# Performance work log

Measured on AMD Instinct MI355X. Metric: run time of the kernel, lower is better.

Reference implementation:

```python
import jax, jax.numpy as jnp
import numpy as np

D_MODEL = 1024
NUM_HEADS = 16


def setup_inputs() -> dict:
    key = jax.random.key(0)
    ks = jax.random.split(key, 5)
    scale = 1.0 / np.sqrt(D_MODEL)
    X = jax.random.normal(ks[0], (4, 2048, D_MODEL), dtype=jnp.float32)
    W_q = jax.random.normal(ks[1], (D_MODEL, D_MODEL), dtype=jnp.float32) * scale
    W_k = jax.random.normal(ks[2], (D_MODEL, D_MODEL), dtype=jnp.float32) * scale
    W_v = jax.random.normal(ks[3], (D_MODEL, D_MODEL), dtype=jnp.float32) * scale
    W_o = jax.random.normal(ks[4], (D_MODEL, D_MODEL), dtype=jnp.float32) * scale
    return {"X": X, "W_q": W_q, "W_k": W_k, "W_v": W_v, "W_o": W_o}


def reference(X, W_q, W_k, W_v, W_o):
    b, s, d_model = X.shape
    h = NUM_HEADS
    d_k = d_model // h
    # Linear projections (y = x @ W^T convention; W stored as [out,in] would be
    # x @ W.T, but with random weights we use x @ W — math is identical in form).
    def split_heads(y):
        return y.reshape(b, s, h, d_k).transpose(0, 2, 1, 3)  # b h s d
    q = split_heads(X @ W_q)
    k = split_heads(X @ W_k)
    v = split_heads(X @ W_v)
    scores = jnp.einsum('bhid,bhjd->bhij', q, k) / jnp.sqrt(jnp.float32(d_k))
    causal = jnp.tril(jnp.ones((s, s), dtype=bool))
    scores = jnp.where(causal[None, None], scores, jnp.float32(-jnp.inf))
    probs = jax.nn.softmax(scores, axis=-1)
    attended = jnp.einsum('bhij,bhjd->bhid', probs, v)
    out = attended.transpose(0, 2, 1, 3).reshape(b, s, d_model)
    return out @ W_o
```

## Files before the change

kernel.cpp:

```cpp
#include <hip/hip_runtime.h>

typedef __bf16 bf16;
typedef __attribute__((ext_vector_type(8))) __bf16 bf16x8;
typedef __attribute__((ext_vector_type(4))) float f32x4;
typedef __attribute__((ext_vector_type(4))) unsigned short u16x4;

#define D_MODEL 1024
#define SEQ     2048
#define NB      4
#define NH      16
#define DK      64
#define MROWS   (NB * SEQ)

#define MFMA_BF16 __builtin_amdgcn_mfma_f32_16x16x32_bf16
#define EXP2F(x) __builtin_amdgcn_exp2f(x)
#define QSCALE 0.18033688011112042f

__device__ __forceinline__ bf16 f2b(float f) {
    union { float f; unsigned u; } c; c.f = f;
    unsigned r = (c.u + 0x7fffu + ((c.u >> 16) & 1u)) >> 16;
    union { unsigned short s; bf16 b; } o; o.s = (unsigned short)r;
    return o.b;
}
__device__ __forceinline__ unsigned short f2u(float f) {
    union { float f; unsigned u; } c; c.f = f;
    return (unsigned short)((c.u + 0x7fffu + ((c.u >> 16) & 1u)) >> 16);
}
__device__ __forceinline__ unsigned fbits(float f) {
    union { float f; unsigned u; } c; c.f = f; return c.u;
}
__device__ __forceinline__ unsigned pack2(float lo, float hi) {
    return __builtin_amdgcn_perm(fbits(hi), fbits(lo), 0x07060302u);
}

template <int N> struct IC { static constexpr int v = N; };

__global__ void prep_kernel(const float* __restrict__ X,
                            const float* __restrict__ Wq, const float* __restrict__ Wk,
                            const float* __restrict__ Wv, const float* __restrict__ Wo,
                            bf16* __restrict__ Xb, bf16* __restrict__ WqkvT,
                            bf16* __restrict__ WoT) {
    __shared__ float tile[32][33];
    const int bid = blockIdx.x;
    if (bid < 8192) {
        int i = bid * 256 + threadIdx.x;
        float4 v = ((const float4*)X)[i];
        u16x4 o; o[0] = f2u(v.x); o[1] = f2u(v.y); o[2] = f2u(v.z); o[3] = f2u(v.w);
        ((u16x4*)Xb)[i] = o;
    } else {
        int r = bid - 8192;
        int w = r >> 10, tl = r & 1023;
        const float* src = (w == 0) ? Wq : (w == 1) ? Wk : (w == 2) ? Wv : Wo;
        bf16* dst = (w == 3) ? WoT : WqkvT + (size_t)w * 1024 * 1024;
        const int n0 = (tl & 31) * 32, k0 = (tl >> 5) * 32;
        const int tx = threadIdx.x & 31, ty = threadIdx.x >> 5;
#pragma unroll
        for (int i = 0; i < 4; i++)
            tile[ty + i * 8][tx] = src[(size_t)(k0 + ty + i * 8) * 1024 + n0 + tx];
        __syncthreads();
#pragma unroll
        for (int i = 0; i < 4; i++)
            dst[(size_t)(n0 + ty + i * 8) * 1024 + k0 + tx] = f2b(tile[tx][ty + i * 8]);
    }
}

__global__ __launch_bounds__(256) void gemm_qkv(const bf16* __restrict__ A,
                                                const bf16* __restrict__ Bt,
                                                bf16* __restrict__ outQ,
                                                bf16* __restrict__ outV) {
    __shared__ __align__(16) bf16 lA[128 * 64];
    __shared__ __align__(16) bf16 lB[128 * 64];

    const int t = threadIdx.x;
    const int wid = t >> 6, lane = t & 63;
    const int ln = lane & 15, qd = lane >> 4;
    const int wm = wid >> 1, wn = wid & 1;

    const int bid = blockIdx.x;
    const int idx = bid >> 3;
    const int colb = (bid & 7) * 3 + (idx % 3);
    const int rowb = idx / 3;
    const int row0 = rowb * 128, col0 = colb * 128;
    const bool isQK = (col0 < 2048);

    const int srow = t >> 3;
    const int schunk = (t & 7) ^ (srow & 7);
    const bf16* ga = A  + (size_t)(row0 + srow) * 1024 + schunk * 8;
    const bf16* gb = Bt + (size_t)(col0 + srow) * 1024 + schunk * 8;
    const int swk = ln & 7;

    f32x4 acc[4][4];
#pragma unroll
    for (int i = 0; i < 4; i++)
#pragma unroll
        for (int j = 0; j < 4; j++) acc[i][j] = (f32x4){0.f, 0.f, 0.f, 0.f};

    for (int kb = 0; kb < 1024; kb += 64) {
#pragma unroll
        for (int c = 0; c < 4; c++) {
            __builtin_amdgcn_global_load_lds(
                (const __attribute__((address_space(1))) void*)(ga + kb + (size_t)c * 32 * 1024),
                (__attribute__((address_space(3))) void*)(&lA[t * 8 + c * 2048]), 16, 0, 0);
            __builtin_amdgcn_global_load_lds(
                (const __attribute__((address_space(1))) void*)(gb + kb + (size_t)c * 32 * 1024),
                (__attribute__((address_space(3))) void*)(&lB[t * 8 + c * 2048]), 16, 0, 0);
        }
        __syncthreads();

#pragma unroll
        for (int ks = 0; ks < 2; ks++) {
            bf16x8 af[4], bfr[4];
#pragma unroll
            for (int i = 0; i < 4; i++)
                af[i] = *(const bf16x8*)&lA[(wm * 64 + i * 16 + ln) * 64
                                            + ((ks * 4 + qd) ^ swk) * 8];
#pragma unroll
            for (int j = 0; j < 4; j++)
                bfr[j] = *(const bf16x8*)&lB[(wn * 64 + j * 16 + ln) * 64
                                             + ((ks * 4 + qd) ^ swk) * 8];
            if (isQK) {
#pragma unroll
                for (int i = 0; i < 4; i++)
#pragma unroll
                    for (int j = 0; j < 4; j++)
                        acc[i][j] = MFMA_BF16(bfr[j], af[i], acc[i][j], 0, 0, 0);
            } else {
#pragma unroll
                for (int i = 0; i < 4; i++)
#pragma unroll
                    for (int j = 0; j < 4; j++)
                        acc[i][j] = MFMA_BF16(af[i], bfr[j], acc[i][j], 0, 0, 0);
            }
        }
        __syncthreads();
    }

    if (isQK) {
#pragma unroll
        for (int i = 0; i < 4; i++)
#pragma unroll
            for (int j = 0; j < 4; j++) {
                int m  = row0 + wm * 64 + i * 16 + ln;
                int n0 = col0 + wn * 64 + j * 16 + qd * 4;
                float scale = (n0 < 1024) ? QSCALE : 1.0f;
                int b = m >> 11, s = m & 2047;
                int h = (n0 & 1023) >> 6, d0 = n0 & 63;
                size_t addr = (((size_t)(b * NH + h) * SEQ + s) * DK + d0)
                              + (size_t)(n0 >> 10) * 8388608;
                u16x4 w;
#pragma unroll
                for (int r = 0; r < 4; r++) w[r] = f2u(acc[i][j][r] * scale);
                *(u16x4*)&outQ[addr] = w;
            }
    } else {
#pragma unroll
        for (int i = 0; i < 4; i++)
#pragma unroll
            for (int j = 0; j < 4; j++) {
                int m0 = row0 + wm * 64 + i * 16 + qd * 4;
                int n  = col0 + wn * 64 + j * 16 + ln - 2048;
                int b = m0 >> 11, s0 = m0 & 2047;
                int h = n >> 6, d = n & 63;
                size_t addr = ((size_t)(b * NH + h) * DK + d) * SEQ + s0;
                u16x4 w;
#pragma unroll
                for (int r = 0; r < 4; r++) w[r] = f2u(acc[i][j][r]);
                *(u16x4*)&outV[addr] = w;
            }
    }
}

__global__ __launch_bounds__(256) void gemm_o(const bf16* __restrict__ A,
                                              const bf16* __restrict__ Bt,
                                              float* __restrict__ out) {
    __shared__ __align__(16) bf16 lA[128 * 64];
    __shared__ __align__(16) bf16 lB[128 * 64];

    const int t = threadIdx.x;
    const int wid = t >> 6, lane = t & 63;
    const int ln = lane & 15, qd = lane >> 4;
    const int wm = wid >> 1, wn = wid & 1;

    const int bid = blockIdx.x;
    const int colb = bid & 7, rowb = bid >> 3;
    const int row0 = rowb * 128, col0 = colb * 128;

    const int srow = t >> 3;
    const int schunk = (t & 7) ^ (srow & 7);
    const bf16* ga = A  + (size_t)(row0 + srow) * 1024 + schunk * 8;
    const bf16* gb = Bt + (size_t)(col0 + srow) * 1024 + schunk * 8;
    const int swk = ln & 7;

    f32x4 acc[4][4];
#pragma unroll
    for (int i = 0; i < 4; i++)
#pragma unroll
        for (int j = 0; j < 4; j++) acc[i][j] = (f32x4){0.f, 0.f, 0.f, 0.f};

    for (int kb = 0; kb < 1024; kb += 64) {
#pragma unroll
        for (int c = 0; c < 4; c++) {
            __builtin_amdgcn_global_load_lds(
                (const __attribute__((address_space(1))) void*)(ga + kb + (size_t)c * 32 * 1024),
                (__attribute__((address_space(3))) void*)(&lA[t * 8 + c * 2048]), 16, 0, 0);
            __builtin_amdgcn_global_load_lds(
                (const __attribute__((address_space(1))) void*)(gb + kb + (size_t)c * 32 * 1024),
                (__attribute__((address_space(3))) void*)(&lB[t * 8 + c * 2048]), 16, 0, 0);
        }
        __syncthreads();

#pragma unroll
        for (int ks = 0; ks < 2; ks++) {
            bf16x8 af[4], bfr[4];
#pragma unroll
            for (int i = 0; i < 4; i++)
                af[i] = *(const bf16x8*)&lA[(wm * 64 + i * 16 + ln) * 64
                                            + ((ks * 4 + qd) ^ swk) * 8];
#pragma unroll
            for (int j = 0; j < 4; j++)
                bfr[j] = *(const bf16x8*)&lB[(wn * 64 + j * 16 + ln) * 64
                                             + ((ks * 4 + qd) ^ swk) * 8];
#pragma unroll
            for (int i = 0; i < 4; i++)
#pragma unroll
                for (int j = 0; j < 4; j++)
                    acc[i][j] = MFMA_BF16(bfr[j], af[i], acc[i][j], 0, 0, 0);
        }
        __syncthreads();
    }

#pragma unroll
    for (int i = 0; i < 4; i++)
#pragma unroll
        for (int j = 0; j < 4; j++) {
            int m  = row0 + wm * 64 + i * 16 + ln;
            int n0 = col0 + wn * 64 + j * 16 + qd * 4;
            *(f32x4*)&out[(size_t)m * 1024 + n0] = acc[i][j];
        }
}

__global__ __launch_bounds__(256) void attn_kernel(const bf16* __restrict__ Q,
                                                   const bf16* __restrict__ K,
                                                   const bf16* __restrict__ Vt,
                                                   bf16* __restrict__ attn_out) {
    __shared__ __align__(16) bf16 kbuf[2][64 * 64];
    __shared__ __align__(16) bf16 vbuf[2][64 * 64];
    __shared__ __align__(16) bf16 plds[4][16 * 64];

    const int t = threadIdx.x;
    const int wid = t >> 6, lane = t & 63;
    const int ln = lane & 15, qd = lane >> 4;

    const int bid = blockIdx.x;
    const int bh   = ((bid >> 7) << 3) | (bid & 7);
    const int pair = (bid >> 3) & 15;
    const int gA = pair, gB = 31 - pair;
    const int ntA = gA + 1, ntT = 33;

    const bf16* Qh = Q  + (size_t)bh * SEQ * DK;
    const bf16* Kh = K  + (size_t)bh * SEQ * DK;
    const bf16* Vh = Vt + (size_t)bh * DK * SEQ;
    bf16* pw = &plds[wid][0];

    const int srow = t >> 3;
    const int schunk = (t & 7) ^ (srow & 7);
    const bf16* kgp = Kh + (size_t)srow * DK + schunk * 8;
    const bf16* vgp = Vh + (size_t)srow * SEQ + schunk * 8;
    const int swk = ln & 7;

    f32x4 o[4];
    float l;
    int qw0;
    bf16x8 qf0, qf1;

    auto stage = [&](int kb, int buf) {
#pragma unroll
        for (int c = 0; c < 2; c++) {
            __builtin_amdgcn_global_load_lds(
                (const __attribute__((address_space(1))) void*)(kgp + (size_t)(kb + c * 32) * DK),
                (__attribute__((address_space(3))) void*)(&kbuf[buf][t * 8 + c * 2048]), 16, 0, 0);
            __builtin_amdgcn_global_load_lds(
                (const __attribute__((address_space(1))) void*)(vgp + (size_t)c * 32 * SEQ + kb),
                (__attribute__((address_space(3))) void*)(&vbuf[buf][t * 8 + c * 2048]), 16, 0, 0);
        }
    };
    auto initGroup = [&](int g) {
        qw0 = g * 64 + wid * 16;
        qf0 = *(const bf16x8*)(Qh + (size_t)(qw0 + ln) * DK + qd * 8);
        qf1 = *(const bf16x8*)(Qh + (size_t)(qw0 + ln) * DK + 32 + qd * 8);
#pragma unroll
        for (int c = 0; c < 4; c++) o[c] = (f32x4){0.f, 0.f, 0.f, 0.f};
        l = 0.f;
    };
    const int b = bh >> 4, h = bh & 15;
    auto finalize = [&]() {
        float ll = l;
        ll += __shfl_xor(ll, 16);
        ll += __shfl_xor(ll, 32);
        float inv = 1.0f / ll;
        size_t orow = ((size_t)(b * SEQ + qw0 + ln)) * D_MODEL + h * DK;
#pragma unroll
        for (int c = 0; c < 4; c++) {
            u16x4 w;
#pragma unroll
            for (int r = 0; r < 4; r++) w[r] = f2u(o[c][r] * inv);
            *(u16x4*)&attn_out[orow + c * 16 + qd * 4] = w;
        }
    };

    auto step = [&](auto curc, int i) {
        constexpr int CUR = decltype(curc)::v;
        __syncthreads();
        int nx = i + 1;
        if (nx < ntT) {
            int kbn = ((nx < ntA) ? nx : nx - ntA) * 64;
            stage(kbn, CUR ^ 1);
        }
        const int kb = ((i < ntA) ? i : i - ntA) * 64;
        const int nkk = min(4, max(0, ((qw0 + 15 - kb) >> 4) + 1));

        if (nkk > 0) {
            f32x4 st[4];
#pragma unroll
            for (int kk = 0; kk < 4; kk++)
                if (kk < nkk) {
                    const bf16* base = &kbuf[CUR][(kk * 16 + ln) * 64];
                    bf16x8 kf0 = *(const bf16x8*)(base + ((qd    ) ^ swk) * 8);
                    bf16x8 kf1 = *(const bf16x8*)(base + ((qd + 4) ^ swk) * 8);
                    f32x4 z = (f32x4){0.f, 0.f, 0.f, 0.f};
                    st[kk] = MFMA_BF16(kf0, qf0, z, 0, 0, 0);
                    st[kk] = MFMA_BF16(kf1, qf1, st[kk], 0, 0, 0);
                }

            float ps = 0.f;
#pragma unroll
            for (int kk = 0; kk < 4; kk++) {
                unsigned pk0 = 0, pk1 = 0;
                if (kk < nkk) {
                    f32x4 s = st[kk];
                    if (kb + kk * 16 == qw0) {
#pragma unroll
                        for (int r = 0; r < 4; r++)
                            if (qd * 4 + r > ln) s[r] = -INFINITY;
                    }
                    float p0 = EXP2F(s[0]);
                    float p1 = EXP2F(s[1]);
                    float p2 = EXP2F(s[2]);
                    float p3 = EXP2F(s[3]);
                    ps += (p0 + p1) + (p2 + p3);
                    pk0 = pack2(p0, p1);
                    pk1 = pack2(p2, p3);
                }
                int cw = 2 * kk + (qd >> 1);
                *(uint2*)&pw[ln * 64 + (cw ^ swk) * 8 + (qd & 1) * 4] =
                    make_uint2(pk0, pk1);
            }
            l += ps;

            asm volatile("s_waitcnt lgkmcnt(0)" ::: "memory");

#pragma unroll
            for (int half = 0; half < 2; half++)
                if (half == 0 || nkk > 2) {
                    bf16x8 pa = *(const bf16x8*)&pw[ln * 64 + ((half * 4 + qd) ^ swk) * 8];
#pragma unroll
                    for (int c = 0; c < 4; c++) {
                        bf16x8 vf = *(const bf16x8*)&vbuf[CUR][(c * 16 + ln) * 64
                                        + ((half * 4 + qd) ^ swk) * 8];
                        o[c] = MFMA_BF16(vf, pa, o[c], 0, 0, 0);
                    }
                }
        }

        if (i == ntA - 1) { finalize(); initGroup(gB); }
    };

    stage(0, 0);
    initGroup(gA);

    step(IC<0>{}, 0);
    for (int ii = 0; ii < 16; ii++) {
        step(IC<1>{}, 2 * ii + 1);
        step(IC<0>{}, 2 * ii + 2);
    }
    finalize();
}

extern "C" void kernel_launch(void* const* d_in, const int* in_sizes, int n_in,
                              void* d_out, int out_size, void* d_ws, size_t ws_size,
                              hipStream_t stream) {
    const float* X  = (const float*)d_in[0];
    const float* Wq = (const float*)d_in[1];
    const float* Wk = (const float*)d_in[2];
    const float* Wv = (const float*)d_in[3];
    const float* Wo = (const float*)d_in[4];
    float* out = (float*)d_out;
    char* ws = (char*)d_ws;

    bf16* Xb    = (bf16*)(ws);
    bf16* WqkvT = (bf16*)(ws + (16u << 20));
    bf16* WoT   = (bf16*)(ws + (22u << 20));
    bf16* Qb    = (bf16*)(ws + (24u << 20));
    bf16* Vt    = (bf16*)(ws + (56u << 20));
    bf16* Attn  = Xb;
    bf16* Kb    = Qb + (size_t)8388608;

    prep_kernel<<<dim3(12288), dim3(256), 0, stream>>>(X, Wq, Wk, Wv, Wo,
                                                       Xb, WqkvT, WoT);

    gemm_qkv<<<dim3(1536), dim3(256), 0, stream>>>(Xb, WqkvT, Qb, Vt);

    attn_kernel<<<dim3(1024), dim3(256), 0, stream>>>(Qb, Kb, Vt, Attn);

    gemm_o<<<dim3(512), dim3(256), 0, stream>>>(Attn, WoT, out);
}
```

Measured before the change: 253.8 us.

## Rewrite causal attention with 32x32 MFMA tiles and register-resident P

The attention kernel now uses 32x32x16 bf16 MFMAs, with each wave handling 32 query rows, so one block covers 128 queries. The old scheme paired two 64-row groups per block; now each block covers one 128-row group and the grid is ordered largest-first. The probability tile no longer goes through LDS: P is packed with v_cvt_pk_bf16_f32 and rearranged across lanes with permlane32_swap to feed the PV MFMA directly. s_setprio hints and launch_bounds(256,3) are added. The aim is to cut LDS traffic, waitcnt stalls and MFMA issue overhead, at the cost of more registers per wave and blocks with uneven amounts of work.

After: 257.2 us. Within noise of the previous version (+1.3%).

```diff
diff --git a/kernel.cpp b/kernel.cpp
--- a/kernel.cpp
+++ b/kernel.cpp
@@ -3,7 +3,9 @@
 typedef __bf16 bf16;
 typedef __attribute__((ext_vector_type(8))) __bf16 bf16x8;
 typedef __attribute__((ext_vector_type(4))) float f32x4;
+typedef __attribute__((ext_vector_type(16))) float f32x16;
 typedef __attribute__((ext_vector_type(4))) unsigned short u16x4;
+typedef __attribute__((ext_vector_type(2))) int v2i;
 
 #define D_MODEL 1024
 #define SEQ     2048
@@ -13,6 +15,7 @@
 #define MROWS   (NB * SEQ)
 
 #define MFMA_BF16 __builtin_amdgcn_mfma_f32_16x16x32_bf16
+#define MFMA32    __builtin_amdgcn_mfma_f32_32x32x16_bf16
 #define EXP2F(x) __builtin_amdgcn_exp2f(x)
 #define QSCALE 0.18033688011112042f
 
@@ -26,11 +29,11 @@
     union { float f; unsigned u; } c; c.f = f;
     return (unsigned short)((c.u + 0x7fffu + ((c.u >> 16) & 1u)) >> 16);
 }
-__device__ __forceinline__ unsigned fbits(float f) {
-    union { float f; unsigned u; } c; c.f = f; return c.u;
-}
-__device__ __forceinline__ unsigned pack2(float lo, float hi) {
-    return __builtin_amdgcn_perm(fbits(hi), fbits(lo), 0x07060302u);
+
+__device__ __forceinline__ f32x16 zero16() {
+    f32x16 z = {0.f,0.f,0.f,0.f,0.f,0.f,0.f,0.f,
+                0.f,0.f,0.f,0.f,0.f,0.f,0.f,0.f};
+    return z;
 }
 
 template <int N> struct IC { static constexpr int v = N; };
@@ -239,151 +242,158 @@
         }
 }
 
-__global__ __launch_bounds__(256) void attn_kernel(const bf16* __restrict__ Q,
-                                                   const bf16* __restrict__ K,
-                                                   const bf16* __restrict__ Vt,
-                                                   bf16* __restrict__ attn_out) {
-    __shared__ __align__(16) bf16 kbuf[2][64 * 64];
-    __shared__ __align__(16) bf16 vbuf[2][64 * 64];
-    __shared__ __align__(16) bf16 plds[4][16 * 64];
+__global__ __launch_bounds__(256, 3) void attn_kernel(const bf16* __restrict__ Q,
+                                                      const bf16* __restrict__ K,
+                                                      const bf16* __restrict__ Vt,
+                                                      bf16* __restrict__ attn_out) {
+    __shared__ __align__(16) bf16 smem[4][64 * 64];
 
     const int t = threadIdx.x;
     const int wid = t >> 6, lane = t & 63;
-    const int ln = lane & 15, qd = lane >> 4;
+    const int qcol = lane & 31, h = lane >> 5;
 
     const int bid = blockIdx.x;
-    const int bh   = ((bid >> 7) << 3) | (bid & 7);
-    const int pair = (bid >> 3) & 15;
-    const int gA = pair, gB = 31 - pair;
-    const int ntA = gA + 1, ntT = 33;
+    const int bh = ((bid >> 7) << 3) | (bid & 7);
+    const int g  = 15 - ((bid >> 3) & 15);
+    const int nsteps = 2 * g + 2;
 
     const bf16* Qh = Q  + (size_t)bh * SEQ * DK;
     const bf16* Kh = K  + (size_t)bh * SEQ * DK;
     const bf16* Vh = Vt + (size_t)bh * DK * SEQ;
-    bf16* pw = &plds[wid][0];
+
+    const int qw0 = g * 128 + wid * 32;
 
     const int srow = t >> 3;
     const int schunk = (t & 7) ^ (srow & 7);
     const bf16* kgp = Kh + (size_t)srow * DK + schunk * 8;
     const bf16* vgp = Vh + (size_t)srow * SEQ + schunk * 8;
-    const int swk = ln & 7;
-
-    f32x4 o[4];
-    float l;
-    int qw0;
-    bf16x8 qf0, qf1;
+
+    const char* sbase = (const char*)&smem[0][0];
+    int raddr[4];
+#pragma unroll
+    for (int tt = 0; tt < 4; tt++)
+        raddr[tt] = qcol * 128 + (((2 * tt + h) ^ (lane & 7)) * 16);
+
+    bf16x8 qf[4];
+#pragma unroll
+    for (int tt = 0; tt < 4; tt++)
+        qf[tt] = *(const bf16x8*)(Qh + (size_t)(qw0 + qcol) * DK + tt * 16 + h * 8);
+
+    f32x16 o[2];
+    o[0] = zero16(); o[1] = zero16();
+    float l = 0.f;
 
     auto stage = [&](int kb, int buf) {
 #pragma unroll
         for (int c = 0; c < 2; c++) {
             __builtin_amdgcn_global_load_lds(
                 (const __attribute__((address_space(1))) void*)(kgp + (size_t)(kb + c * 32) * DK),
-                (__attribute__((address_space(3))) void*)(&kbuf[buf][t * 8 + c * 2048]), 16, 0, 0);
+                (__attribute__((address_space(3))) void*)(&smem[buf][t * 8 + c * 2048]), 16, 0, 0);
             __builtin_amdgcn_global_load_lds(
                 (const __attribute__((address_space(1))) void*)(vgp + (size_t)c * 32 * SEQ + kb),
-                (__attribute__((address_space(3))) void*)(&vbuf[buf][t * 8 + c * 2048]), 16, 0, 0);
-        }
-    };
-    auto initGroup = [&](int g) {
-        qw0 = g * 64 + wid * 16;
-        qf0 = *(const bf16x8*)(Qh + (size_t)(qw0 + ln) * DK + qd * 8);
-        qf1 = *(const bf16x8*)(Qh + (size_t)(qw0 + ln) * DK + 32 + qd * 8);
-#pragma unroll
-        for (int c = 0; c < 4; c++) o[c] = (f32x4){0.f, 0.f, 0.f, 0.f};
-        l = 0.f;
-    };
-    const int b = bh >> 4, h = bh & 15;
-    auto finalize = [&]() {
-        float ll = l;
-        ll += __shfl_xor(ll, 16);
-        ll += __shfl_xor(ll, 32);
-        float inv = 1.0f / ll;
-        size_t orow = ((size_t)(b * SEQ + qw0 + ln)) * D_MODEL + h * DK;
-#pragma unroll
-        for (int c = 0; c < 4; c++) {
-            u16x4 w;
-#pragma unroll
-            for (int r = 0; r < 4; r++) w[r] = f2u(o[c][r] * inv);
-            *(u16x4*)&attn_out[orow + c * 16 + qd * 4] = w;
+                (__attribute__((address_space(3))) void*)(&smem[2 + buf][t * 8 + c * 2048]), 16, 0, 0);
         }
     };
 
     auto step = [&](auto curc, int i) {
         constexpr int CUR = decltype(curc)::v;
         __syncthreads();
-        int nx = i + 1;
-        if (nx < ntT) {
-            int kbn = ((nx < ntA) ? nx : nx - ntA) * 64;
-            stage(kbn, CUR ^ 1);
-        }
-        const int kb = ((i < ntA) ? i : i - ntA) * 64;
-        const int nkk = min(4, max(0, ((qw0 + 15 - kb) >> 4) + 1));
-
-        if (nkk > 0) {
-            f32x4 st[4];
-#pragma unroll
-            for (int kk = 0; kk < 4; kk++)
-                if (kk < nkk) {
-                    const bf16* base = &kbuf[CUR][(kk * 16 + ln) * 64];
-                    bf16x8 kf0 = *(const bf16x8*)(base + ((qd    ) ^ swk) * 8);
-                    bf16x8 kf1 = *(const bf16x8*)(base + ((qd + 4) ^ swk) * 8);
-                    f32x4 z = (f32x4){0.f, 0.f, 0.f, 0.f};
-                    st[kk] = MFMA_BF16(kf0, qf0, z, 0, 0, 0);
-                    st[kk] = MFMA_BF16(kf1, qf1, st[kk], 0, 0, 0);
+        const int nx = i + 1;
+        if (nx < nsteps) stage(nx * 64, CUR ^ 1);
+        const int kb = i * 64;
+        const int nt = min(2, max(0, ((qw0 + 31 - kb) >> 5) + 1));
+        if (nt > 0) {
+            f32x16 st[2];
+            __builtin_amdgcn_s_setprio(1);
+#pragma unroll
+            for (int n = 0; n < 2; n++)
+                if (n < nt) {
+                    f32x16 z = zero16();
+#pragma unroll
+                    for (int tt = 0; tt < 4; tt++) {
+                        bf16x8 kf = *(const bf16x8*)(sbase + raddr[tt]
+                                        + (CUR * 8192 + n * 4096));
+                        z = MFMA32(kf, qf[tt], z, 0, 0, 0);
+                    }
+                    st[n] = z;
                 }
+            __builtin_amdgcn_s_setprio(0);
 
             float ps = 0.f;
 #pragma unroll
-            for (int kk = 0; kk < 4; kk++) {
-                unsigned pk0 = 0, pk1 = 0;
-                if (kk < nkk) {
-                    f32x4 s = st[kk];
-                    if (kb + kk * 16 == qw0) {
-#pragma unroll
-                        for (int r = 0; r < 4; r++)
-                            if (qd * 4 + r > ln) s[r] = -INFINITY;
+            for (int n = 0; n < 2; n++)
+                if (n < nt) {
+                    const bool diag = (kb + 32 * n == qw0);
+#pragma unroll
+                    for (int r = 0; r < 16; r++) {
+                        float pv = EXP2F(st[n][r]);
+                        if (diag) {
+                            const int kloc = (r & 3) + 8 * (r >> 2) + 4 * h;
+                            pv = (kloc > qcol) ? 0.f : pv;
+                        }
+                        st[n][r] = pv;
                     }
-                    float p0 = EXP2F(s[0]);
-                    float p1 = EXP2F(s[1]);
-                    float p2 = EXP2F(s[2]);
-                    float p3 = EXP2F(s[3]);
-                    ps += (p0 + p1) + (p2 + p3);
-                    pk0 = pack2(p0, p1);
-                    pk1 = pack2(p2, p3);
+                    float s0 = (st[n][0] + st[n][1]) + (st[n][2] + st[n][3]);
+                    float s1 = (st[n][4] + st[n][5]) + (st[n][6] + st[n][7]);
+                    float s2 = (st[n][8] + st[n][9]) + (st[n][10] + st[n][11]);
+                    float s3 = (st[n][12] + st[n][13]) + (st[n][14] + st[n][15]);
+                    ps += (s0 + s1) + (s2 + s3);
                 }
-                int cw = 2 * kk + (qd >> 1);
-                *(uint2*)&pw[ln * 64 + (cw ^ swk) * 8 + (qd & 1) * 4] =
-                    make_uint2(pk0, pk1);
-            }
             l += ps;
 
-            asm volatile("s_waitcnt lgkmcnt(0)" ::: "memory");
-
-#pragma unroll
-            for (int half = 0; half < 2; half++)
-                if (half == 0 || nkk > 2) {
-                    bf16x8 pa = *(const bf16x8*)&pw[ln * 64 + ((half * 4 + qd) ^ swk) * 8];
-#pragma unroll
-                    for (int c = 0; c < 4; c++) {
-                        bf16x8 vf = *(const bf16x8*)&vbuf[CUR][(c * 16 + ln) * 64
-                                        + ((half * 4 + qd) ^ swk) * 8];
-                        o[c] = MFMA_BF16(vf, pa, o[c], 0, 0, 0);
+#pragma unroll
+            for (int ks = 0; ks < 4; ks++)
+                if (ks < 2 * nt) {
+                    const int n = ks >> 1, b8 = (ks & 1) * 8;
+                    unsigned A, B, C, D;
+                    asm("v_cvt_pk_bf16_f32 %0, %1, %2"
+                        : "=v"(A) : "v"(st[n][b8 + 0]), "v"(st[n][b8 + 1]));
+                    asm("v_cvt_pk_bf16_f32 %0, %1, %2"
+                        : "=v"(B) : "v"(st[n][b8 + 2]), "v"(st[n][b8 + 3]));
+                    asm("v_cvt_pk_bf16_f32 %0, %1, %2"
+                        : "=v"(C) : "v"(st[n][b8 + 4]), "v"(st[n][b8 + 5]));
+                    asm("v_cvt_pk_bf16_f32 %0, %1, %2"
+                        : "=v"(D) : "v"(st[n][b8 + 6]), "v"(st[n][b8 + 7]));
+                    v2i r02 = __builtin_amdgcn_permlane32_swap((int)A, (int)C, false, false);
+                    v2i r13 = __builtin_amdgcn_permlane32_swap((int)B, (int)D, false, false);
+                    union { unsigned u[4]; bf16x8 v; } pf;
+                    pf.u[0] = (unsigned)r02[0];
+                    pf.u[1] = (unsigned)r13[0];
+                    pf.u[2] = (unsigned)r02[1];
+                    pf.u[3] = (unsigned)r13[1];
+                    __builtin_amdgcn_s_setprio(1);
+#pragma unroll
+                    for (int m = 0; m < 2; m++) {
+                        bf16x8 vf = *(const bf16x8*)(sbase + raddr[ks]
+                                        + (16384 + CUR * 8192 + m * 4096));
+                        o[m] = MFMA32(vf, pf.v, o[m], 0, 0, 0);
                     }
+                    __builtin_amdgcn_s_setprio(0);
                 }
         }
-
-        if (i == ntA - 1) { finalize(); initGroup(gB); }
     };
 
     stage(0, 0);
-    initGroup(gA);
-
     step(IC<0>{}, 0);
-    for (int ii = 0; ii < 16; ii++) {
+    for (int ii = 0; ii < g; ii++) {
         step(IC<1>{}, 2 * ii + 1);
         step(IC<0>{}, 2 * ii + 2);
     }
-    finalize();
+    step(IC<1>{}, 2 * g + 1);
+
+    l += __shfl_xor(l, 32);
+    const float inv = 1.0f / l;
+    const int b = bh >> 4, head = bh & 15;
+    const size_t orow = ((size_t)(b * SEQ + qw0 + qcol)) * D_MODEL + head * DK;
+#pragma unroll
+    for (int m = 0; m < 2; m++)
+#pragma unroll
+        for (int q4 = 0; q4 < 4; q4++) {
+            u16x4 w;
+#pragma unroll
+            for (int c = 0; c < 4; c++) w[c] = f2u(o[m][q4 * 4 + c] * inv);
+            *(u16x4*)&attn_out[orow + m * 32 + q4 * 8 + h * 4] = w;
+        }
 }
 
 extern "C" void kernel_launch(void* const* d_in, const int* in_sizes, int n_in,
```
